# Kernel tuning notes

Hardware: AMD Instinct MI355X
Metric: run time of the kernel (lower is better)

Reference implementation:

```python
import jax, jax.numpy as jnp
import numpy as np

N, E, D_IN, H, C = 50000, 800000, 128, 4, 64
BN_EPS = 1e-5
NEG_SLOPE = 0.2  # PyG GATConv default


def gat_conv(x, edge_index, W, a_src, a_dst, b, heads, out_c):
    """PyG-style GATConv (add_self_loops=True, concat=True, eval mode)."""
    n = x.shape[0]
    loop = jnp.arange(n)
    src = jnp.concatenate([edge_index[0], loop])
    dst = jnp.concatenate([edge_index[1], loop])
    h = (x @ W.T).reshape(n, heads, out_c)  # [N,H,C]
    # per-node attention partials, gathered per edge
    e = (h * a_src).sum(-1)[src] + (h * a_dst).sum(-1)[dst]  # [E+N,H]
    e = jax.nn.leaky_relu(e, NEG_SLOPE)
    # segment softmax over incoming edges of each destination node
    m = jax.ops.segment_max(e, dst, num_segments=n)
    ex = jnp.exp(e - m[dst])
    denom = jax.ops.segment_sum(ex, dst, num_segments=n)
    alpha = ex / (denom[dst] + 1e-16)  # [E+N,H]
    out = jax.ops.segment_sum(h[src] * alpha[:, :, None], dst, num_segments=n)
    return out.reshape(n, heads * out_c) + b


def setup_inputs() -> dict:
    key = jax.random.key(0)
    ks = jax.random.split(key, 24)
    s = 0.05
    inp = {}
    inp['x'] = jax.random.normal(ks[0], (N, D_IN), jnp.float32)
    inp['edge_index'] = jax.random.randint(ks[1], (2, E), 0, N, dtype=jnp.int64)
    # layer 1: in=D_IN, out=C, heads=H
    inp['W1'] = jax.random.normal(ks[2], (H * C, D_IN), jnp.float32) * s
    inp['a_src1'] = jax.random.normal(ks[3], (H, C), jnp.float32) * s
    inp['a_dst1'] = jax.random.normal(ks[4], (H, C), jnp.float32) * s
    inp['b1'] = jnp.zeros((H * C,), jnp.float32)
    # layer 2: in=H*C, out=C, heads=H
    inp['W2'] = jax.random.normal(ks[5], (H * C, H * C), jnp.float32) * s
    inp['a_src2'] = jax.random.normal(ks[6], (H, C), jnp.float32) * s
    inp['a_dst2'] = jax.random.normal(ks[7], (H, C), jnp.float32) * s
    inp['b2'] = jnp.zeros((H * C,), jnp.float32)
    # layer 3: in=H*C, out=1, heads=1
    inp['W3'] = jax.random.normal(ks[8], (1, H * C), jnp.float32) * s
    inp['a_src3'] = jax.random.normal(ks[9], (1, 1), jnp.float32) * s
    inp['a_dst3'] = jax.random.normal(ks[10], (1, 1), jnp.float32) * s
    inp['b3'] = jnp.zeros((1,), jnp.float32)
    # batchnorms (eval mode; running_mean=0, running_var=1 at init)
    inp['bn1_g'] = jnp.ones((H * C,), jnp.float32)
    inp['bn1_b'] = jnp.zeros((H * C,), jnp.float32)
    inp['bn2_g'] = jnp.ones((H * C,), jnp.float32)
    inp['bn2_b'] = jnp.zeros((H * C,), jnp.float32)
    # classifier: Linear(1,64) -> ReLU -> Linear(64,1) -> Sigmoid
    inp['cW1'] = jax.random.normal(ks[11], (C, 1), jnp.float32) * s
    inp['cb1'] = jnp.zeros((C,), jnp.float32)
    inp['cW2'] = jax.random.normal(ks[12], (1, C), jnp.float32) * s
    inp['cb2'] = jnp.zeros((1,), jnp.float32)
    return inp


def reference(x, edge_index, W1, a_src1, a_dst1, b1, W2, a_src2, a_dst2, b2,
              W3, a_src3, a_dst3, b3, bn1_g, bn1_b, bn2_g, bn2_b,
              cW1, cb1, cW2, cb2):
    inv = np.float32(1.0 / np.sqrt(1.0 + BN_EPS))  # eval BN with init running stats
    h = gat_conv(x, edge_index, W1, a_src1, a_dst1, b1, H, C)
    h = jax.nn.relu(bn1_g * h * inv + bn1_b)
    h = gat_conv(h, edge_index, W2, a_src2, a_dst2, b2, H, C)
    h = jax.nn.relu(bn2_g * h * inv + bn2_b)
    h = gat_conv(h, edge_index, W3, a_src3, a_dst3, b3, 1, 1)  # [N,1]
    p = jnp.mean(h, axis=0, keepdims=True)  # [1,1]
    p = jax.nn.relu(p @ cW1.T + cb1)
    p = jax.nn.sigmoid(p @ cW2.T + cb2)
    return p
```

## Files before the change

kernel.cpp:

```cpp
#include <hip/hip_runtime.h>
#include <math.h>

#define NN 50000
#define NE 800000
#define HC 256
#define NHEAD 4
#define MAXD 64

typedef __attribute__((ext_vector_type(8))) short short8;
typedef __attribute__((ext_vector_type(4))) float f32x4;
typedef __attribute__((ext_vector_type(2))) float f32x2;

__device__ __forceinline__ float lrelu(float x){ return x >= 0.f ? x : 0.2f*x; }

__device__ __forceinline__ unsigned short f2bf(float f){
    unsigned int u = __float_as_uint(f);
    unsigned int r = (u + 0x7fffu + ((u >> 16) & 1u)) >> 16;
    return (unsigned short)r;
}

__device__ __forceinline__ void gload_lds16(const void* g, void* l){
    __builtin_amdgcn_global_load_lds(
        (const __attribute__((address_space(1))) void*)g,
        (__attribute__((address_space(3))) void*)l,
        16, 0, 0);
}

__device__ __forceinline__ void cvt4(const float* __restrict__ in, unsigned short* __restrict__ out, int i){
    float4 v = reinterpret_cast<const float4*>(in)[i];
    ushort4 o;
    o.x = f2bf(v.x); o.y = f2bf(v.y); o.z = f2bf(v.z); o.w = f2bf(v.w);
    reinterpret_cast<ushort4*>(out)[i] = o;
}

__global__ void k_cvt3(const float* __restrict__ x,  unsigned short* __restrict__ xb,
                       const float* __restrict__ W1, unsigned short* __restrict__ W1b,
                       const float* __restrict__ W2, unsigned short* __restrict__ W2b,
                       int* __restrict__ cnt){
    const int N1 = NN*128/4, N2 = HC*128/4, N3 = HC*HC/4;
    int i = blockIdx.x*blockDim.x + threadIdx.x;
    if (i < N1) cvt4(x, xb, i);
    else if (i < N1+N2) cvt4(W1, W1b, i-N1);
    else if (i < N1+N2+N3) cvt4(W2, W2b, i-N1-N2);
    if (i < NN) cnt[i] = 0;
}

__global__ __launch_bounds__(256) void k_fillF(const int* __restrict__ ei, int* __restrict__ cnt,
                                               unsigned short* __restrict__ csrF){
    int cls = blockIdx.x & 7;
    int nb  = gridDim.x >> 3;
    int bi  = blockIdx.x >> 3;
    int stride = nb * blockDim.x;
    for (int i = bi*blockDim.x + threadIdx.x; i < NE; i += stride){
        int d = ei[NE + i];
        if (((d >> 6) & 7) == cls){
            int s = ei[i];
            int slot = atomicAdd(&cnt[d], 1);
            if (slot < MAXD) csrF[(size_t)d*MAXD + slot] = (unsigned short)s;
        }
    }
}

template<int K>
__global__ __launch_bounds__(256) void k_gemm_mfma(const unsigned short* __restrict__ A,
                                                   const unsigned short* __restrict__ W,
                                                   unsigned char* __restrict__ C8,
                                                   const float* __restrict__ asrc,
                                                   const float* __restrict__ adst,
                                                   float* __restrict__ as_,
                                                   float* __restrict__ ad_){
    __shared__ unsigned short As[2][128*64];
    __shared__ unsigned short Bs[2][128*64];

    int tid  = threadIdx.x;
    int wid  = tid >> 6, lane = tid & 63;
    int rb   = blockIdx.x >> 1;
    int cb   = blockIdx.x & 1;
    int row0 = rb*128, col0 = cb*128;
    int wr   = wid >> 1, wc = wid & 1;
    int frow = lane & 15, kg = lane >> 4;
    const int NT = K/64;

    int srow = (wid<<3) + (lane>>3);
    int sg   = (lane&7) ^ ((lane>>3)&7);

    f32x4 acc[4][4];
    #pragma unroll
    for (int m=0;m<4;m++)
        #pragma unroll
        for (int n=0;n<4;n++){ acc[m][n][0]=0.f; acc[m][n][1]=0.f; acc[m][n][2]=0.f; acc[m][n][3]=0.f; }

    auto STAGE = [&](int buf, int kt){
        #pragma unroll
        for (int i=0;i<4;i++){
            int r = i*32 + srow;
            gload_lds16(&A[(size_t)(row0 + r)*K + kt*64 + sg*8],
                        (void*)&As[buf][(i*32 + (wid<<3))*64]);
        }
        #pragma unroll
        for (int i=0;i<4;i++){
            int c = i*32 + srow;
            gload_lds16(&W[(size_t)(col0 + c)*K + kt*64 + sg*8],
                        (void*)&Bs[buf][(i*32 + (wid<<3))*64]);
        }
    };

    auto COMPUTE = [&](int buf){
        #pragma unroll
        for (int ks=0; ks<2; ks++){
            short8 a[4], b[4];
            int pg = ((ks<<2)|kg) ^ (frow&7);
            #pragma unroll
            for (int m=0;m<4;m++){
                int row = wr*64 + m*16 + frow;
                a[m] = *reinterpret_cast<const short8*>(&As[buf][row*64 + pg*8]);
            }
            #pragma unroll
            for (int n=0;n<4;n++){
                int col = wc*64 + n*16 + frow;
                b[n] = *reinterpret_cast<const short8*>(&Bs[buf][col*64 + pg*8]);
            }
            #pragma unroll
            for (int m=0;m<4;m++)
                #pragma unroll
                for (int n=0;n<4;n++)
                    acc[m][n] = __builtin_amdgcn_mfma_f32_16x16x32_bf16(a[m], b[n], acc[m][n], 0, 0, 0);
        }
    };

    STAGE(0, 0);
    __syncthreads();
    for (int kt = 0; kt < NT; ++kt){
        int cur = kt & 1;
        if (kt+1 < NT) STAGE(cur^1, kt+1);
        COMPUTE(cur);
        __syncthreads();
    }

    int crow = kg*4;
    int ccol = lane & 15;
    int wrow0 = row0 + wr*64, wcol0 = col0 + wc*64;
    #pragma unroll
    for (int m=0;m<4;m++){
        #pragma unroll
        for (int q=0;q<4;q++){
            int gr = wrow0 + m*16 + crow + q;
            if (gr < NN){
                int v01 = __builtin_amdgcn_cvt_pk_fp8_f32(acc[m][0][q], acc[m][1][q], 0, false);
                int v23 = __builtin_amdgcn_cvt_pk_fp8_f32(acc[m][2][q], acc[m][3][q], 0, false);
                size_t base = (size_t)gr*HC + wcol0 + ccol;
                C8[base +  0] = (unsigned char)( v01        & 0xff);
                C8[base + 16] = (unsigned char)((v01 >> 8)  & 0xff);
                C8[base + 32] = (unsigned char)( v23        & 0xff);
                C8[base + 48] = (unsigned char)((v23 >> 8)  & 0xff);
            }
        }
    }

    int hw = (wcol0 >> 6) & 3;
    float as_r[4], ad_r[4];
    #pragma unroll
    for (int n=0;n<4;n++){
        int ch = hw*64 + n*16 + ccol;
        as_r[n] = asrc[ch];
        ad_r[n] = adst[ch];
    }
    #pragma unroll
    for (int m=0;m<4;m++){
        #pragma unroll
        for (int q=0;q<4;q++){
            float ps=0.f, pd=0.f;
            #pragma unroll
            for (int n=0;n<4;n++){
                float v = acc[m][n][q];
                ps += v * as_r[n];
                pd += v * ad_r[n];
            }
            #pragma unroll
            for (int off=1; off<16; off<<=1){
                ps += __shfl_xor(ps, off);
                pd += __shfl_xor(pd, off);
            }
            int gr = wrow0 + m*16 + crow + q;
            if (ccol==0 && gr < NN){
                as_[gr*NHEAD + hw] = ps;
                ad_[gr*NHEAD + hw] = pd;
            }
        }
    }
}

__global__ __launch_bounds__(256) void k_aggw(
        const unsigned char* __restrict__ hlin8, const float* __restrict__ as_, const float* __restrict__ ad_,
        const int* __restrict__ cnt, const unsigned short* __restrict__ csrF,
        const float* __restrict__ bias, const float* __restrict__ bn_g, const float* __restrict__ bn_b,
        unsigned short* __restrict__ outb, const float* __restrict__ W3, float* __restrict__ h3){
    int lane = threadIdx.x & 63;
    int n = blockIdx.x*4 + (threadIdx.x >> 6);
    if (n >= NN) return;
    int h  = lane >> 4;
    int el = lane & 15;
    int hb = lane & 48;
    int deg = min(cnt[n], MAXD);

    float adh = ad_[n*NHEAD + h];
    float swt = __expf(lrelu(as_[n*NHEAD + h] + adh));

    const unsigned int* row8 = (const unsigned int*)hlin8;
    float a0=0.f, a1=0.f, a2=0.f, a3=0.f;
    float dsum = 0.f;

    for (int c0 = 0; c0 < deg; c0 += 16){
        int nc = min(16, deg - c0);
        int s = n; float wt = 0.f;
        if (el < nc){
            s = (int)csrF[(size_t)n*MAXD + c0 + el];
            wt = __expf(lrelu(as_[s*NHEAD + h] + adh));
        }
        dsum += wt;
        for (int e0 = 0; e0 < nc; e0 += 4){
            float w0 = __shfl(wt, hb | (e0+0));
            float w1 = __shfl(wt, hb | (e0+1));
            float w2 = __shfl(wt, hb | (e0+2));
            float w3v= __shfl(wt, hb | (e0+3));
            int   s0 = __shfl(s, e0+0);
            int   s1 = __shfl(s, e0+1);
            int   s2 = __shfl(s, e0+2);
            int   s3 = __shfl(s, e0+3);
            unsigned int u0 = row8[(size_t)s0*64 + lane];
            unsigned int u1 = row8[(size_t)s1*64 + lane];
            unsigned int u2 = row8[(size_t)s2*64 + lane];
            unsigned int u3 = row8[(size_t)s3*64 + lane];
            f32x2 p0a = __builtin_amdgcn_cvt_pk_f32_fp8((int)u0, false);
            f32x2 p0b = __builtin_amdgcn_cvt_pk_f32_fp8((int)u0, true);
            f32x2 p1a = __builtin_amdgcn_cvt_pk_f32_fp8((int)u1, false);
            f32x2 p1b = __builtin_amdgcn_cvt_pk_f32_fp8((int)u1, true);
            f32x2 p2a = __builtin_amdgcn_cvt_pk_f32_fp8((int)u2, false);
            f32x2 p2b = __builtin_amdgcn_cvt_pk_f32_fp8((int)u2, true);
            f32x2 p3a = __builtin_amdgcn_cvt_pk_f32_fp8((int)u3, false);
            f32x2 p3b = __builtin_amdgcn_cvt_pk_f32_fp8((int)u3, true);
            a0 += w0*p0a[0]; a1 += w0*p0a[1]; a2 += w0*p0b[0]; a3 += w0*p0b[1];
            a0 += w1*p1a[0]; a1 += w1*p1a[1]; a2 += w1*p1b[0]; a3 += w1*p1b[1];
            a0 += w2*p2a[0]; a1 += w2*p2a[1]; a2 += w2*p2b[0]; a3 += w2*p2b[1];
            a0 += w3v*p3a[0]; a1 += w3v*p3a[1]; a2 += w3v*p3b[0]; a3 += w3v*p3b[1];
        }
    }

    #pragma unroll
    for (int off=1; off<16; off<<=1) dsum += __shfl_xor(dsum, off);
    float dinv = 1.f / (dsum + swt + 1e-16f);

    unsigned int su = row8[(size_t)n*64 + lane];
    f32x2 sa = __builtin_amdgcn_cvt_pk_f32_fp8((int)su, false);
    f32x2 sb = __builtin_amdgcn_cvt_pk_f32_fp8((int)su, true);
    a0 += swt*sa[0]; a1 += swt*sa[1]; a2 += swt*sb[0]; a3 += swt*sb[1];

    const float bninv = rsqrtf(1.f + 1e-5f);
    float4 bi = ((const float4*)bias)[lane];
    float4 gg = ((const float4*)bn_g)[lane];
    float4 bb = ((const float4*)bn_b)[lane];
    float v0 = fmaxf(gg.x*bninv*(a0*dinv + bi.x) + bb.x, 0.f);
    float v1 = fmaxf(gg.y*bninv*(a1*dinv + bi.y) + bb.y, 0.f);
    float v2 = fmaxf(gg.z*bninv*(a2*dinv + bi.z) + bb.z, 0.f);
    float v3 = fmaxf(gg.w*bninv*(a3*dinv + bi.w) + bb.w, 0.f);

    if (outb){
        uint2 o;
        o.x = ((unsigned int)f2bf(v1) << 16) | (unsigned int)f2bf(v0);
        o.y = ((unsigned int)f2bf(v3) << 16) | (unsigned int)f2bf(v2);
        ((uint2*)outb)[(size_t)n*64 + lane] = o;
    }

    if (W3){
        float4 w3 = ((const float4*)W3)[lane];
        float p3 = v0*w3.x + v1*w3.y + v2*w3.z + v3*w3.w;
        #pragma unroll
        for (int off=32; off; off>>=1) p3 += __shfl_xor(p3, off);
        if (lane == 0) h3[n] = p3;
    }
}

__global__ __launch_bounds__(256) void k_agg3(const float* __restrict__ h3,
        const int* __restrict__ cnt, const unsigned short* __restrict__ csrF,
        const float* __restrict__ a_src3, const float* __restrict__ a_dst3, const float* __restrict__ b3,
        float* __restrict__ nodeout){
    int lane = threadIdx.x & 63;
    int n = blockIdx.x*4 + (threadIdx.x >> 6);
    if (n >= NN) return;
    float As3 = a_src3[0], Ad3 = a_dst3[0];
    int deg = min(cnt[n], MAXD);
    float hn = h3[n];
    float adn = hn*Ad3;
    float eself = lrelu(hn*As3 + adn);
    float s = (lane==0)? __expf(eself) : 0.f;
    float o = (lane==0)? __expf(eself)*hn : 0.f;
    if (lane < deg){
        float hs = h3[(int)csrF[(size_t)n*MAXD + lane]];
        float wv = __expf(lrelu(hs*As3 + adn));
        s += wv; o += wv*hs;
    }
    #pragma unroll
    for (int off=32; off; off>>=1){ s += __shfl_xor(s, off); o += __shfl_xor(o, off); }
    if (lane==0) nodeout[n] = o/(s+1e-16f) + b3[0];
}

__global__ __launch_bounds__(1024) void k_finred(const float* __restrict__ nodeout,
        const float* __restrict__ cW1, const float* __restrict__ cb1,
        const float* __restrict__ cW2, const float* __restrict__ cb2, float* __restrict__ out){
    int t = threadIdx.x;
    float v = 0.f;
    for (int j = t; j < NN; j += 1024) v += nodeout[j];
    #pragma unroll
    for (int off=32; off; off>>=1) v += __shfl_xor(v, off);
    __shared__ float red[16];
    if ((t&63)==0) red[t>>6] = v;
    __syncthreads();
    if (t < 64){
        float p = 0.f;
        #pragma unroll
        for (int i=0;i<16;i++) p += red[i];
        p /= (float)NN;
        float z1 = fmaxf(p * cW1[t] + cb1[t], 0.f);
        float vv = z1 * cW2[t];
        #pragma unroll
        for (int off=32; off; off>>=1) vv += __shfl_xor(vv, off);
        if (t==0) out[0] = 1.f/(1.f+__expf(-(vv + cb2[0])));
    }
}

extern "C" void kernel_launch(void* const* d_in, const int* in_sizes, int n_in,
                              void* d_out, int out_size, void* d_ws, size_t ws_size,
                              hipStream_t stream){
    const float* x      = (const float*)d_in[0];
    const int*   ei     = (const int*)  d_in[1];
    const float* W1     = (const float*)d_in[2];
    const float* a_src1 = (const float*)d_in[3];
    const float* a_dst1 = (const float*)d_in[4];
    const float* b1     = (const float*)d_in[5];
    const float* W2     = (const float*)d_in[6];
    const float* a_src2 = (const float*)d_in[7];
    const float* a_dst2 = (const float*)d_in[8];
    const float* b2     = (const float*)d_in[9];
    const float* W3     = (const float*)d_in[10];
    const float* a_src3 = (const float*)d_in[11];
    const float* a_dst3 = (const float*)d_in[12];
    const float* b3     = (const float*)d_in[13];
    const float* bn1_g  = (const float*)d_in[14];
    const float* bn1_b  = (const float*)d_in[15];
    const float* bn2_g  = (const float*)d_in[16];
    const float* bn2_b  = (const float*)d_in[17];
    const float* cW1    = (const float*)d_in[18];
    const float* cb1    = (const float*)d_in[19];
    const float* cW2    = (const float*)d_in[20];
    const float* cb2    = (const float*)d_in[21];

    char* p = (char*)d_ws;
    unsigned char*  hlin8 = (unsigned char*)p;  p += (size_t)NN*HC;
    unsigned short* featb = (unsigned short*)p; p += (size_t)NN*HC*2;
    unsigned short* xb    = (unsigned short*)p; p += (size_t)NN*128*2;
    unsigned short* W1b   = (unsigned short*)p; p += (size_t)HC*128*2;
    unsigned short* W2b   = (unsigned short*)p; p += (size_t)HC*HC*2;
    float* as_  = (float*)p;  p += (size_t)NN*NHEAD*4;
    float* ad_  = (float*)p;  p += (size_t)NN*NHEAD*4;
    float* h3   = (float*)p;  p += (size_t)NN*4;
    float* nodeout = (float*)p; p += (size_t)NN*4;
    int* cnt    = (int*)p;    p += (size_t)NN*4;
    unsigned short* csrF = (unsigned short*)p; p += (size_t)NN*MAXD*2;

    const int NCVT = NN*128/4 + HC*128/4 + HC*HC/4;
    k_cvt3<<<(NCVT + 255)/256, 256, 0, stream>>>(x, xb, W1, W1b, W2, W2b, cnt);

    k_fillF<<<3128, 256, 0, stream>>>(ei, cnt, csrF);

    const int GB = ((NN + 127)/128) * 2;

    k_gemm_mfma<128><<<GB, 256, 0, stream>>>(xb, W1b, hlin8, a_src1, a_dst1, as_, ad_);
    k_aggw<<<(NN+3)/4, 256, 0, stream>>>(hlin8, as_, ad_, cnt, csrF, b1, bn1_g, bn1_b, featb, nullptr, nullptr);

    k_gemm_mfma<256><<<GB, 256, 0, stream>>>(featb, W2b, hlin8, a_src2, a_dst2, as_, ad_);
    k_aggw<<<(NN+3)/4, 256, 0, stream>>>(hlin8, as_, ad_, cnt, csrF, b2, bn2_g, bn2_b, nullptr, W3, h3);

    k_agg3<<<(NN+3)/4, 256, 0, stream>>>(h3, cnt, csrF, a_src3, a_dst3, b3, nodeout);
    k_finred<<<1, 1024, 0, stream>>>(nodeout, cW1, cb1, cW2, cb2, (float*)d_out);
}
```

Before: 201.2 us.

## Merge CSR fill and first GEMM into one kernel launch to overlap them

The CSR fill and the layer-1 GEMM are independent, so they now run in one grid: the first blocks do the atomic edge fill and the remaining blocks do the MFMA GEMM. This removes a kernel boundary and lets the latency-bound atomic scatter share the GPU with the compute-bound GEMM. The cost is that every fill block now reserves the GEMM's 64 KB of static LDS, which may limit how many fill blocks fit on a CU at once.

```diff
diff --git a/kernel.cpp b/kernel.cpp
--- a/kernel.cpp
+++ b/kernel.cpp
@@ -6,6 +6,7 @@
 #define HC 256
 #define NHEAD 4
 #define MAXD 64
+#define FILLB 3128
 
 typedef __attribute__((ext_vector_type(8))) short short8;
 typedef __attribute__((ext_vector_type(4))) float f32x4;
@@ -45,13 +46,13 @@
     if (i < NN) cnt[i] = 0;
 }
 
-__global__ __launch_bounds__(256) void k_fillF(const int* __restrict__ ei, int* __restrict__ cnt,
-                                               unsigned short* __restrict__ csrF){
-    int cls = blockIdx.x & 7;
-    int nb  = gridDim.x >> 3;
-    int bi  = blockIdx.x >> 3;
-    int stride = nb * blockDim.x;
-    for (int i = bi*blockDim.x + threadIdx.x; i < NE; i += stride){
+__device__ __forceinline__ void fill_body(int bid, const int* __restrict__ ei,
+                                          int* __restrict__ cnt, unsigned short* __restrict__ csrF){
+    int cls = bid & 7;
+    int nb  = FILLB >> 3;
+    int bi  = bid >> 3;
+    int stride = nb * 256;
+    for (int i = bi*256 + threadIdx.x; i < NE; i += stride){
         int d = ei[NE + i];
         if (((d >> 6) & 7) == cls){
             int s = ei[i];
@@ -62,20 +63,20 @@
 }
 
 template<int K>
-__global__ __launch_bounds__(256) void k_gemm_mfma(const unsigned short* __restrict__ A,
-                                                   const unsigned short* __restrict__ W,
-                                                   unsigned char* __restrict__ C8,
-                                                   const float* __restrict__ asrc,
-                                                   const float* __restrict__ adst,
-                                                   float* __restrict__ as_,
-                                                   float* __restrict__ ad_){
-    __shared__ unsigned short As[2][128*64];
-    __shared__ unsigned short Bs[2][128*64];
-
+__device__ __forceinline__ void gemm_body(int bid,
+                                          unsigned short* __restrict__ As,
+                                          unsigned short* __restrict__ Bs,
+                                          const unsigned short* __restrict__ A,
+                                          const unsigned short* __restrict__ W,
+                                          unsigned char* __restrict__ C8,
+                                          const float* __restrict__ asrc,
+                                          const float* __restrict__ adst,
+                                          float* __restrict__ as_,
+                                          float* __restrict__ ad_){
     int tid  = threadIdx.x;
     int wid  = tid >> 6, lane = tid & 63;
-    int rb   = blockIdx.x >> 1;
-    int cb   = blockIdx.x & 1;
+    int rb   = bid >> 1;
+    int cb   = bid & 1;
     int row0 = rb*128, col0 = cb*128;
     int wr   = wid >> 1, wc = wid & 1;
     int frow = lane & 15, kg = lane >> 4;
@@ -95,13 +96,13 @@
         for (int i=0;i<4;i++){
             int r = i*32 + srow;
             gload_lds16(&A[(size_t)(row0 + r)*K + kt*64 + sg*8],
-                        (void*)&As[buf][(i*32 + (wid<<3))*64]);
+                        (void*)&As[buf*8192 + (i*32 + (wid<<3))*64]);
         }
         #pragma unroll
         for (int i=0;i<4;i++){
             int c = i*32 + srow;
             gload_lds16(&W[(size_t)(col0 + c)*K + kt*64 + sg*8],
-                        (void*)&Bs[buf][(i*32 + (wid<<3))*64]);
+                        (void*)&Bs[buf*8192 + (i*32 + (wid<<3))*64]);
         }
     };
 
@@ -113,12 +114,12 @@
             #pragma unroll
             for (int m=0;m<4;m++){
                 int row = wr*64 + m*16 + frow;
-                a[m] = *reinterpret_cast<const short8*>(&As[buf][row*64 + pg*8]);
+                a[m] = *reinterpret_cast<const short8*>(&As[buf*8192 + row*64 + pg*8]);
             }
             #pragma unroll
             for (int n=0;n<4;n++){
                 int col = wc*64 + n*16 + frow;
-                b[n] = *reinterpret_cast<const short8*>(&Bs[buf][col*64 + pg*8]);
+                b[n] = *reinterpret_cast<const short8*>(&Bs[buf*8192 + col*64 + pg*8]);
             }
             #pragma unroll
             for (int m=0;m<4;m++)
@@ -188,6 +189,36 @@
             }
         }
     }
+}
+
+__global__ __launch_bounds__(256) void k_fill_gemm1(const int* __restrict__ ei,
+                                                    int* __restrict__ cnt, unsigned short* __restrict__ csrF,
+                                                    const unsigned short* __restrict__ A,
+                                                    const unsigned short* __restrict__ W,
+                                                    unsigned char* __restrict__ C8,
+                                                    const float* __restrict__ asrc,
+                                                    const float* __restrict__ adst,
+                                                    float* __restrict__ as_,
+                                                    float* __restrict__ ad_){
+    __shared__ unsigned short As[2*128*64];
+    __shared__ unsigned short Bs[2*128*64];
+    if (blockIdx.x < FILLB){
+        fill_body(blockIdx.x, ei, cnt, csrF);
+    } else {
+        gemm_body<128>(blockIdx.x - FILLB, As, Bs, A, W, C8, asrc, adst, as_, ad_);
+    }
+}
+
+__global__ __launch_bounds__(256) void k_gemm2(const unsigned short* __restrict__ A,
+                                               const unsigned short* __restrict__ W,
+                                               unsigned char* __restrict__ C8,
+                                               const float* __restrict__ asrc,
+                                               const float* __restrict__ adst,
+                                               float* __restrict__ as_,
+                                               float* __restrict__ ad_){
+    __shared__ unsigned short As[2*128*64];
+    __shared__ unsigned short Bs[2*128*64];
+    gemm_body<256>(blockIdx.x, As, Bs, A, W, C8, asrc, adst, as_, ad_);
 }
 
 __global__ __launch_bounds__(256) void k_aggw(
@@ -370,14 +401,13 @@
     const int NCVT = NN*128/4 + HC*128/4 + HC*HC/4;
     k_cvt3<<<(NCVT + 255)/256, 256, 0, stream>>>(x, xb, W1, W1b, W2, W2b, cnt);
 
-    k_fillF<<<3128, 256, 0, stream>>>(ei, cnt, csrF);
-
     const int GB = ((NN + 127)/128) * 2;
 
-    k_gemm_mfma<128><<<GB, 256, 0, stream>>>(xb, W1b, hlin8, a_src1, a_dst1, as_, ad_);
+    k_fill_gemm1<<<FILLB + GB, 256, 0, stream>>>(ei, cnt, csrF,
+                                                 xb, W1b, hlin8, a_src1, a_dst1, as_, ad_);
     k_aggw<<<(NN+3)/4, 256, 0, stream>>>(hlin8, as_, ad_, cnt, csrF, b1, bn1_g, bn1_b, featb, nullptr, nullptr);
 
-    k_gemm_mfma<256><<<GB, 256, 0, stream>>>(featb, W2b, hlin8, a_src2, a_dst2, as_, ad_);
+    k_gemm2<<<GB, 256, 0, stream>>>(featb, W2b, hlin8, a_src2, a_dst2, as_, ad_);
     k_aggw<<<(NN+3)/4, 256, 0, stream>>>(hlin8, as_, ad_, cnt, csrF, b2, bn2_g, bn2_b, nullptr, W3, h3);
 
     k_agg3<<<(NN+3)/4, 256, 0, stream>>>(h3, cnt, csrF, a_src3, a_dst3, b3, nodeout);
```

After: 205.4 us. 1.02x slower.
